# Optimization experiments

Hardware: AMD Instinct MI355X
Metric: run time of the kernel (lower is better)

Reference implementation:

```python
import jax, jax.numpy as jnp
from jax import lax
import numpy as np

B, T, F = 2048, 256, 64
HIDDEN = [64, 32, 16]
OUT = 1


def _lstm_params(key, in_dim, h):
    k1, k2, k3 = jax.random.split(key, 3)
    s_in = 1.0 / np.sqrt(in_dim)
    s_h = 1.0 / np.sqrt(h)
    W = jax.random.uniform(k1, (in_dim, 4 * h), jnp.float32, -s_in, s_in)
    U = jax.random.uniform(k2, (h, 4 * h), jnp.float32, -s_h, s_h)
    # Keras unit_forget_bias: bias starts at 0 except forget gate = 1
    b = jnp.concatenate([jnp.zeros((h,)), jnp.ones((h,)), jnp.zeros((2 * h,))]).astype(jnp.float32)
    return W, U, b


def setup_inputs() -> dict:
    key = jax.random.key(0)
    ks = jax.random.split(key, 6)
    x = jax.random.normal(ks[0], (B, T, F), jnp.float32)
    W0, U0, b0 = _lstm_params(ks[1], F, HIDDEN[0])
    W1, U1, b1 = _lstm_params(ks[2], HIDDEN[0], HIDDEN[1])
    W2, U2, b2 = _lstm_params(ks[3], HIDDEN[1], HIDDEN[2])
    s = 1.0 / np.sqrt(HIDDEN[2])
    Wd = jax.random.uniform(ks[4], (HIDDEN[2], OUT), jnp.float32, -s, s)
    bd = jnp.zeros((OUT,), jnp.float32)
    return {"x": x, "W0": W0, "U0": U0, "b0": b0,
            "W1": W1, "U1": U1, "b1": b1,
            "W2": W2, "U2": U2, "b2": b2,
            "Wd": Wd, "bd": bd}


def _lstm(x, W, U, b):
    """Keras-style LSTM scan. x: [B,T,in]. Returns (seq [B,T,H], last_h [B,H]).
    Gate order i,f,g,o; recurrent_activation=sigmoid, activation=tanh.
    Dropout/recurrent_dropout are identity at inference (training=False)."""
    Bsz = x.shape[0]
    H = U.shape[0]
    # precompute input projection for all timesteps (one big GEMM)
    xz = jnp.einsum('bti,ig->btg', x, W) + b  # [B,T,4H]
    xz_t = jnp.swapaxes(xz, 0, 1)  # [T,B,4H]

    def step(carry, z_in):
        h, c = carry
        z = z_in + h @ U  # [B,4H]
        i, f, g, o = jnp.split(z, 4, axis=-1)
        i = jax.nn.sigmoid(i)
        f = jax.nn.sigmoid(f)
        g = jnp.tanh(g)
        o = jax.nn.sigmoid(o)
        c = f * c + i * g
        h = o * jnp.tanh(c)
        return (h, c), h

    init = (jnp.zeros((Bsz, H), x.dtype), jnp.zeros((Bsz, H), x.dtype))
    (h_last, _), hs = lax.scan(step, init, xz_t)
    return jnp.swapaxes(hs, 0, 1), h_last


def reference(x, W0, U0, b0, W1, U1, b1, W2, U2, b2, Wd, bd):
    h, _ = _lstm(x, W0, U0, b0)          # return_sequences=True -> [B,T,64]
    h, _ = _lstm(h, W1, U1, b1)          # return_sequences=True -> [B,T,32]
    _, h_last = _lstm(h, W2, U2, b2)     # return_sequences=False -> [B,16]
    return h_last @ Wd + bd              # Dense -> [B,1]
```

## Files before the change

### kernel.cpp

```cpp
#include <hip/hip_runtime.h>


typedef __attribute__((ext_vector_type(8))) short s8v;
typedef __attribute__((ext_vector_type(4))) float f4v;
typedef unsigned short ushort_t;

#define T_STEPS 256
#define BT 8

#define XH  0
#define XL  2048
#define H0H 4096
#define H0L 6144
#define H1H 8192
#define H1L 9216
#define H2H 10240
#define H2L 11264
#define SM_SHORTS 12288

#define PIN(v) asm volatile("" : "+v"(v))
#define BAR()  asm volatile("s_waitcnt lgkmcnt(0)\n\ts_barrier" ::: "memory")

__device__ __forceinline__ unsigned short f2bf(float f) {
    unsigned u = __float_as_uint(f);
    u += 0x7fff + ((u >> 16) & 1);
    return (unsigned short)(u >> 16);
}
__device__ __forceinline__ float bf2f(unsigned short s) {
    return __uint_as_float(((unsigned)s) << 16);
}
__device__ __forceinline__ void tsplit(float v, unsigned short& hi, unsigned short& lo) {
    unsigned u = __float_as_uint(v);
    hi = (unsigned short)(u >> 16);
    float r = v - __uint_as_float(u & 0xffff0000u);
    lo = (unsigned short)(__float_as_uint(r) >> 16);
}
__device__ __forceinline__ float sigmoid_f(float x) {
    return __builtin_amdgcn_rcpf(1.0f + __expf(-x));
}
__device__ __forceinline__ float tanh_f(float x) {
    return 1.0f - 2.0f * __builtin_amdgcn_rcpf(__expf(2.0f * x) + 1.0f);
}

__device__ __forceinline__ float wval(const float* W, const float* U,
                                      int inDim, int KH, int fourH, int k, int n) {
    if (k < inDim) return W[k * fourH + n];
    if (k < KH)    return U[(k - inDim) * fourH + n];
    return 0.0f;
}
__device__ __forceinline__ void load_bfrag(const float* W, const float* U,
                                           int inDim, int KH, int fourH,
                                           int k0, int n, s8v& hi, s8v& lo) {
#pragma unroll
    for (int j = 0; j < 8; ++j) {
        float w = wval(W, U, inDim, KH, fourH, k0 + j, n);
        unsigned short h = f2bf(w);
        unsigned short l = f2bf(w - bf2f(h));
        hi[j] = (short)h;
        lo[j] = (short)l;
    }
}

__device__ __forceinline__ void gates2(const f4v* acc, bool low, float* c, float* hn) {
#pragma unroll
    for (int j = 0; j < 2; ++j) {
        float si = __shfl_xor(acc[0][j + 2], 32);
        float sf = __shfl_xor(acc[1][j + 2], 32);
        float sg = __shfl_xor(acc[2][j + 2], 32);
        float so = __shfl_xor(acc[3][j + 2], 32);
        float zi = low ? acc[0][j] : si;
        float zf = low ? acc[1][j] : sf;
        float zg = low ? acc[2][j] : sg;
        float zo = low ? acc[3][j] : so;
        float ig = sigmoid_f(zi);
        float fg = sigmoid_f(zf);
        float gg = tanh_f(zg);
        float og = sigmoid_f(zo);
        c[j] = fmaf(fg, c[j], ig * gg);
        hn[j] = og * tanh_f(c[j]);
    }
}

__global__ __attribute__((amdgpu_flat_work_group_size(512, 512),
                          amdgpu_waves_per_eu(2, 2)))
void lstm_pipe(const float* __restrict__ x,
               const float* __restrict__ W0, const float* __restrict__ U0, const float* __restrict__ b0,
               const float* __restrict__ W1, const float* __restrict__ U1, const float* __restrict__ b1,
               const float* __restrict__ W2, const float* __restrict__ U2, const float* __restrict__ b2,
               const float* __restrict__ Wd, const float* __restrict__ bd,
               float* __restrict__ out)
{
    const int tid  = threadIdx.x;
    const int lane = tid & 63;
    const int wv   = tid >> 6;
    const int fr   = lane >> 4;
    const int fc   = lane & 15;
    const int bbase = blockIdx.x * BT;

    __shared__ __align__(16) ushort_t SMEM[SM_SHORTS];
    __shared__ __align__(16) float h2last[BT][16];

    {
        unsigned* p32 = (unsigned*)SMEM;
        for (int i = tid; i < SM_SHORTS / 2; i += 512) p32[i] = 0u;
    }
    __syncthreads();

    const ushort_t* rb = SMEM + lane * 8;
    const bool low = (lane < 32);
    const int rowb = (fr & 1) * 4 + ((fr >> 1) << 1);

    if (wv < 4) {
        s8v Bh[4][4], Bl[4][4];
        float bias[4];
#pragma unroll
        for (int g = 0; g < 4; ++g) {
            int n = g * 64 + wv * 16 + fc;
            bias[g] = b0[n];
#pragma unroll
            for (int kc = 0; kc < 4; ++kc)
                load_bfrag(W0, U0, 64, 128, 256, kc * 32 + fr * 8, n, Bh[g][kc], Bl[g][kc]);
        }
#pragma unroll
        for (int g = 0; g < 4; ++g) {
            PIN(bias[g]);
#pragma unroll
            for (int kc = 0; kc < 4; ++kc) { PIN(Bh[g][kc]); PIN(Bl[g][kc]); }
        }
        float c0[2] = {0.f, 0.f};
        const int hq  = wv >> 1;
        const int k   = (wv & 1) * 16 + fc;
        const int ibw = (k >> 3) * 128 + (k & 7);
        __syncthreads();
        for (int s = 0; s < T_STEPS + 2; ++s) {
            if (s < T_STEPS) {
                const ushort_t* r = rb + ((s & 1) << 10);
                s8v ah[4], al[4];
                ah[0] = *(const s8v*)&r[XH  +   0];
                al[0] = *(const s8v*)&r[XL  +   0];
                ah[1] = *(const s8v*)&r[XH  + 512];
                al[1] = *(const s8v*)&r[XL  + 512];
                ah[2] = *(const s8v*)&r[H0H +   0];
                al[2] = *(const s8v*)&r[H0L +   0];
                ah[3] = *(const s8v*)&r[H0H + 512];
                al[3] = *(const s8v*)&r[H0L + 512];
                f4v acc[4];
#pragma unroll
                for (int g = 0; g < 4; ++g) acc[g] = (f4v){bias[g], bias[g], bias[g], bias[g]};
#pragma unroll
                for (int kc = 0; kc < 4; ++kc) {
#pragma unroll
                    for (int g = 0; g < 4; ++g)
                        acc[g] = __builtin_amdgcn_mfma_f32_16x16x32_bf16(ah[kc], Bh[g][kc], acc[g], 0, 0, 0);
#pragma unroll
                    for (int g = 0; g < 4; ++g)
                        acc[g] = __builtin_amdgcn_mfma_f32_16x16x32_bf16(al[kc], Bh[g][kc], acc[g], 0, 0, 0);
#pragma unroll
                    for (int g = 0; g < 4; ++g)
                        acc[g] = __builtin_amdgcn_mfma_f32_16x16x32_bf16(ah[kc], Bl[g][kc], acc[g], 0, 0, 0);
                }
                float hn[2];
                gates2(acc, low, c0, hn);
                {
                    ushort_t* w = SMEM + (((s & 1) ^ 1) << 10) + hq * 512 + ibw;
#pragma unroll
                    for (int j = 0; j < 2; ++j) {
                        unsigned short hh_, ll_;
                        tsplit(hn[j], hh_, ll_);
                        w[H0H + (rowb + j) * 8] = hh_;
                        w[H0L + (rowb + j) * 8] = ll_;
                    }
                }
            }
            BAR();
        }
    } else if (wv < 6) {
        s8v Bh[4][3], Bl[4][3];
        float bias[4];
#pragma unroll
        for (int g = 0; g < 4; ++g) {
            int n = g * 32 + (wv & 1) * 16 + fc;
            bias[g] = b1[n];
#pragma unroll
            for (int kc = 0; kc < 3; ++kc)
                load_bfrag(W1, U1, 64, 96, 128, kc * 32 + fr * 8, n, Bh[g][kc], Bl[g][kc]);
        }
#pragma unroll
        for (int g = 0; g < 4; ++g) {
            PIN(bias[g]);
#pragma unroll
            for (int kc = 0; kc < 3; ++kc) { PIN(Bh[g][kc]); PIN(Bl[g][kc]); }
        }
        float c1[2] = {0.f, 0.f};
        const int k   = (wv & 1) * 16 + fc;
        const int ibw = (k >> 3) * 128 + (k & 7);
        __syncthreads();
        for (int s = 0; s < T_STEPS + 2; ++s) {
            if (s >= 1 && s <= T_STEPS) {
                const int p = s & 1;
                const ushort_t* r  = rb + (p << 10);
                const ushort_t* r1 = rb + (p << 9);
                s8v ah[3], al[3];
                ah[0] = *(const s8v*)&r[H0H +   0];
                al[0] = *(const s8v*)&r[H0L +   0];
                ah[1] = *(const s8v*)&r[H0H + 512];
                al[1] = *(const s8v*)&r[H0L + 512];
                ah[2] = *(const s8v*)&r1[H1H];
                al[2] = *(const s8v*)&r1[H1L];
                f4v acc[4];
#pragma unroll
                for (int g = 0; g < 4; ++g) acc[g] = (f4v){bias[g], bias[g], bias[g], bias[g]};
#pragma unroll
                for (int kc = 0; kc < 3; ++kc) {
#pragma unroll
                    for (int g = 0; g < 4; ++g)
                        acc[g] = __builtin_amdgcn_mfma_f32_16x16x32_bf16(ah[kc], Bh[g][kc], acc[g], 0, 0, 0);
#pragma unroll
                    for (int g = 0; g < 4; ++g)
                        acc[g] = __builtin_amdgcn_mfma_f32_16x16x32_bf16(al[kc], Bh[g][kc], acc[g], 0, 0, 0);
#pragma unroll
                    for (int g = 0; g < 4; ++g)
                        acc[g] = __builtin_amdgcn_mfma_f32_16x16x32_bf16(ah[kc], Bl[g][kc], acc[g], 0, 0, 0);
                }
                float hn[2];
                gates2(acc, low, c1, hn);
                {
                    ushort_t* w = SMEM + ((p ^ 1) << 9) + ibw;
#pragma unroll
                    for (int j = 0; j < 2; ++j) {
                        unsigned short hh_, ll_;
                        tsplit(hn[j], hh_, ll_);
                        w[H1H + (rowb + j) * 8] = hh_;
                        w[H1L + (rowb + j) * 8] = ll_;
                    }
                }
            }
            BAR();
        }
    } else if (wv == 6) {
        s8v Bh[4][2], Bl[4][2];
        float bias[4];
#pragma unroll
        for (int g = 0; g < 4; ++g) {
            int n = g * 16 + fc;
            bias[g] = b2[n];
#pragma unroll
            for (int kc = 0; kc < 2; ++kc)
                load_bfrag(W2, U2, 32, 48, 64, kc * 32 + fr * 8, n, Bh[g][kc], Bl[g][kc]);
        }
#pragma unroll
        for (int g = 0; g < 4; ++g) {
            PIN(bias[g]);
#pragma unroll
            for (int kc = 0; kc < 2; ++kc) { PIN(Bh[g][kc]); PIN(Bl[g][kc]); }
        }
        float c2[2] = {0.f, 0.f};
        const int ibw = (fc >> 3) * 128 + (fc & 7);
        __syncthreads();
        for (int s = 0; s < T_STEPS + 2; ++s) {
            if (s >= 2) {
                const int p = s & 1;
                const ushort_t* r1 = rb + (p << 9);
                s8v ah[2], al[2];
                ah[0] = *(const s8v*)&r1[H1H];
                al[0] = *(const s8v*)&r1[H1L];
                ah[1] = *(const s8v*)&r1[H2H];
                al[1] = *(const s8v*)&r1[H2L];
                f4v acc[4];
#pragma unroll
                for (int g = 0; g < 4; ++g) acc[g] = (f4v){bias[g], bias[g], bias[g], bias[g]};
#pragma unroll
                for (int kc = 0; kc < 2; ++kc) {
#pragma unroll
                    for (int g = 0; g < 4; ++g)
                        acc[g] = __builtin_amdgcn_mfma_f32_16x16x32_bf16(ah[kc], Bh[g][kc], acc[g], 0, 0, 0);
#pragma unroll
                    for (int g = 0; g < 4; ++g)
                        acc[g] = __builtin_amdgcn_mfma_f32_16x16x32_bf16(al[kc], Bh[g][kc], acc[g], 0, 0, 0);
#pragma unroll
                    for (int g = 0; g < 4; ++g)
                        acc[g] = __builtin_amdgcn_mfma_f32_16x16x32_bf16(ah[kc], Bl[g][kc], acc[g], 0, 0, 0);
                }
                float hn[2];
                gates2(acc, low, c2, hn);
                {
                    ushort_t* w = SMEM + ((p ^ 1) << 9) + ibw;
#pragma unroll
                    for (int j = 0; j < 2; ++j) {
                        unsigned short hh_, ll_;
                        tsplit(hn[j], hh_, ll_);
                        w[H2H + (rowb + j) * 8] = hh_;
                        w[H2L + (rowb + j) * 8] = ll_;
                    }
                    if (s == T_STEPS + 1) {
#pragma unroll
                        for (int j = 0; j < 2; ++j) h2last[rowb + j][fc] = hn[j];
                    }
                }
            }
            BAR();
        }
    } else {
        const int xb = lane >> 3;
        const int fo = (lane & 7) * 8;
        const float* xp = x + ((size_t)(bbase + xb) * T_STEPS) * 64 + fo;
        const int o2 = (fo >> 5) * 512 + (((fo & 31) >> 3) * 16 + xb) * 8;

        auto write_x = [&](float4 v0, float4 v1, int tt) {
            float vv[8] = {v0.x, v0.y, v0.z, v0.w, v1.x, v1.y, v1.z, v1.w};
            s8v hi8, lo8;
#pragma unroll
            for (int j = 0; j < 8; ++j) {
                unsigned short h_, l_;
                tsplit(vv[j], h_, l_);
                hi8[j] = (short)h_;
                lo8[j] = (short)l_;
            }
            ushort_t* wbp = SMEM + ((tt & 1) << 10) + o2;
            *(s8v*)&wbp[XH] = hi8;
            *(s8v*)&wbp[XL] = lo8;
        };

        float4 pa = *(const float4*)(xp);
        float4 pb = *(const float4*)(xp + 4);
        write_x(pa, pb, 0);
        pa = *(const float4*)(xp + 64);
        pb = *(const float4*)(xp + 64 + 4);
        __syncthreads();
        for (int s = 0; s < T_STEPS + 2; ++s) {
            float4 na, nb;
            const bool ld = (s + 2 < T_STEPS);
            if (ld) {
                na = *(const float4*)(xp + (size_t)(s + 2) * 64);
                nb = *(const float4*)(xp + (size_t)(s + 2) * 64 + 4);
            }
            if (s + 1 < T_STEPS) write_x(pa, pb, s + 1);
            if (ld) { pa = na; pb = nb; }
            BAR();
        }
    }

    __syncthreads();
    if (tid < BT) {
        float acc = bd[0];
#pragma unroll
        for (int j = 0; j < 16; ++j) acc += h2last[tid][j] * Wd[j];
        out[bbase + tid] = acc;
    }
}

extern "C" void kernel_launch(void* const* d_in, const int* in_sizes, int n_in,
                              void* d_out, int out_size, void* d_ws, size_t ws_size,
                              hipStream_t stream) {
    (void)in_sizes; (void)n_in; (void)d_ws; (void)ws_size; (void)out_size;
    const float* x  = (const float*)d_in[0];
    const float* W0 = (const float*)d_in[1];
    const float* U0 = (const float*)d_in[2];
    const float* b0 = (const float*)d_in[3];
    const float* W1 = (const float*)d_in[4];
    const float* U1 = (const float*)d_in[5];
    const float* b1 = (const float*)d_in[6];
    const float* W2 = (const float*)d_in[7];
    const float* U2 = (const float*)d_in[8];
    const float* b2 = (const float*)d_in[9];
    const float* Wd = (const float*)d_in[10];
    const float* bd = (const float*)d_in[11];
    float* out = (float*)d_out;

    dim3 grid(2048 / BT);
    dim3 block(512);
    hipLaunchKernelGGL(lstm_pipe, grid, block, 0, stream,
                       x, W0, U0, b0, W1, U1, b1, W2, U2, b2, Wd, bd, out);
}
```

Measured before the change: 416.6 us.

## Move layer-0 input projection into loader waves, staging gate preactivations in LDS

```diff
diff --git a/kernel.cpp b/kernel.cpp
--- a/kernel.cpp
+++ b/kernel.cpp
@@ -8,15 +8,13 @@
 #define T_STEPS 256
 #define BT 8
 
-#define XH  0
-#define XL  2048
-#define H0H 4096
-#define H0L 6144
-#define H1H 8192
-#define H1L 9216
-#define H2H 10240
-#define H2L 11264
-#define SM_SHORTS 12288
+#define H0H 0
+#define H0L 2048
+#define H1H 4096
+#define H1L 5120
+#define H2H 6144
+#define H2L 7168
+#define SM_SHORTS 8192
 
 #define PIN(v) asm volatile("" : "+v"(v))
 #define BAR()  asm volatile("s_waitcnt lgkmcnt(0)\n\ts_barrier" ::: "memory")
@@ -81,6 +79,32 @@
     }
 }
 
+template<int CG0>
+__device__ __forceinline__ void produce8(const s8v* axh, const s8v* axl,
+                                         const float* bw, int pcpar,
+                                         int lane, int fr, int fc,
+                                         ushort_t* w0s, float* zx)
+{
+    const int woff = (pcpar << 12) + ((fr >> 1) << 11) + ((fr & 1) << 2);
+#pragma unroll
+    for (int i = 0; i < 8; ++i) {
+        const int cg = CG0 + i;
+        const int col = cg * 16 + fc;
+        const float bv = bw[cg];
+        f4v acc = (f4v){bv, bv, bv, bv};
+#pragma unroll
+        for (int kc = 0; kc < 2; ++kc) {
+            const int fb = ((cg * 2 + kc) << 9) + lane * 8;
+            s8v bh = *(const s8v*)&w0s[fb];
+            s8v bl = *(const s8v*)&w0s[16384 + fb];
+            acc = __builtin_amdgcn_mfma_f32_16x16x32_bf16(axh[kc], bh, acc, 0, 0, 0);
+            acc = __builtin_amdgcn_mfma_f32_16x16x32_bf16(axl[kc], bh, acc, 0, 0, 0);
+            acc = __builtin_amdgcn_mfma_f32_16x16x32_bf16(axh[kc], bl, acc, 0, 0, 0);
+        }
+        *(f4v*)&zx[woff + col * 8] = acc;
+    }
+}
+
 __global__ __attribute__((amdgpu_flat_work_group_size(512, 512),
                           amdgpu_waves_per_eu(2, 2)))
 void lstm_pipe(const float* __restrict__ x,
@@ -98,12 +122,25 @@
     const int bbase = blockIdx.x * BT;
 
     __shared__ __align__(16) ushort_t SMEM[SM_SHORTS];
+    __shared__ __align__(16) float    ZX[8192];
+    __shared__ __align__(16) ushort_t W0S[32768];
     __shared__ __align__(16) float h2last[BT][16];
 
     {
         unsigned* p32 = (unsigned*)SMEM;
         for (int i = tid; i < SM_SHORTS / 2; i += 512) p32[i] = 0u;
     }
+    for (int it = tid; it < 16384; it += 512) {
+        const int n = it & 255;
+        const int k = it >> 8;
+        const float w = W0[it];
+        const int kc = k >> 5, kfr = (k >> 3) & 3, j = k & 7;
+        const int cg = n >> 4, nfc = n & 15;
+        const int pos = ((cg * 2 + kc) * 64 + (kfr * 16 + nfc)) * 8 + j;
+        unsigned short h = f2bf(w);
+        W0S[pos] = h;
+        W0S[16384 + pos] = f2bf(w - bf2f(h));
+    }
     __syncthreads();
 
     const ushort_t* rb = SMEM + lane * 8;
@@ -111,54 +148,53 @@
     const int rowb = (fr & 1) * 4 + ((fr >> 1) << 1);
 
     if (wv < 4) {
-        s8v Bh[4][4], Bl[4][4];
-        float bias[4];
+        s8v Bh[4][2], Bl[4][2];
 #pragma unroll
         for (int g = 0; g < 4; ++g) {
             int n = g * 64 + wv * 16 + fc;
-            bias[g] = b0[n];
-#pragma unroll
-            for (int kc = 0; kc < 4; ++kc)
-                load_bfrag(W0, U0, 64, 128, 256, kc * 32 + fr * 8, n, Bh[g][kc], Bl[g][kc]);
-        }
-#pragma unroll
-        for (int g = 0; g < 4; ++g) {
-            PIN(bias[g]);
-#pragma unroll
-            for (int kc = 0; kc < 4; ++kc) { PIN(Bh[g][kc]); PIN(Bl[g][kc]); }
-        }
+#pragma unroll
+            for (int kc = 0; kc < 2; ++kc)
+                load_bfrag(U0, U0, 64, 64, 256, kc * 32 + fr * 8, n, Bh[g][kc], Bl[g][kc]);
+        }
+#pragma unroll
+        for (int g = 0; g < 4; ++g)
+#pragma unroll
+            for (int kc = 0; kc < 2; ++kc) { PIN(Bh[g][kc]); PIN(Bl[g][kc]); }
         float c0[2] = {0.f, 0.f};
         const int hq  = wv >> 1;
         const int k   = (wv & 1) * 16 + fc;
         const int ibw = (k >> 3) * 128 + (k & 7);
+        const int zb  = (wv * 16 + fc) * 8 + ((fr & 1) << 2);
         __syncthreads();
         for (int s = 0; s < T_STEPS + 2; ++s) {
             if (s < T_STEPS) {
                 const ushort_t* r = rb + ((s & 1) << 10);
-                s8v ah[4], al[4];
-                ah[0] = *(const s8v*)&r[XH  +   0];
-                al[0] = *(const s8v*)&r[XL  +   0];
-                ah[1] = *(const s8v*)&r[XH  + 512];
-                al[1] = *(const s8v*)&r[XL  + 512];
-                ah[2] = *(const s8v*)&r[H0H +   0];
-                al[2] = *(const s8v*)&r[H0L +   0];
-                ah[3] = *(const s8v*)&r[H0H + 512];
-                al[3] = *(const s8v*)&r[H0L + 512];
+                s8v ah0 = *(const s8v*)&r[H0H +   0];
+                s8v al0 = *(const s8v*)&r[H0L +   0];
+                s8v ah1 = *(const s8v*)&r[H0H + 512];
+                s8v al1 = *(const s8v*)&r[H0L + 512];
+                const float* zr = ZX + ((((s >> 1) & 1) << 12) + ((s & 1) << 11) + zb);
                 f4v acc[4];
 #pragma unroll
-                for (int g = 0; g < 4; ++g) acc[g] = (f4v){bias[g], bias[g], bias[g], bias[g]};
-#pragma unroll
-                for (int kc = 0; kc < 4; ++kc) {
-#pragma unroll
-                    for (int g = 0; g < 4; ++g)
-                        acc[g] = __builtin_amdgcn_mfma_f32_16x16x32_bf16(ah[kc], Bh[g][kc], acc[g], 0, 0, 0);
-#pragma unroll
-                    for (int g = 0; g < 4; ++g)
-                        acc[g] = __builtin_amdgcn_mfma_f32_16x16x32_bf16(al[kc], Bh[g][kc], acc[g], 0, 0, 0);
-#pragma unroll
-                    for (int g = 0; g < 4; ++g)
-                        acc[g] = __builtin_amdgcn_mfma_f32_16x16x32_bf16(ah[kc], Bl[g][kc], acc[g], 0, 0, 0);
-                }
+                for (int g = 0; g < 4; ++g) acc[g] = *(const f4v*)&zr[g * 512];
+#pragma unroll
+                for (int g = 0; g < 4; ++g)
+                    acc[g] = __builtin_amdgcn_mfma_f32_16x16x32_bf16(ah0, Bh[g][0], acc[g], 0, 0, 0);
+#pragma unroll
+                for (int g = 0; g < 4; ++g)
+                    acc[g] = __builtin_amdgcn_mfma_f32_16x16x32_bf16(al0, Bh[g][0], acc[g], 0, 0, 0);
+#pragma unroll
+                for (int g = 0; g < 4; ++g)
+                    acc[g] = __builtin_amdgcn_mfma_f32_16x16x32_bf16(ah0, Bl[g][0], acc[g], 0, 0, 0);
+#pragma unroll
+                for (int g = 0; g < 4; ++g)
+                    acc[g] = __builtin_amdgcn_mfma_f32_16x16x32_bf16(ah1, Bh[g][1], acc[g], 0, 0, 0);
+#pragma unroll
+                for (int g = 0; g < 4; ++g)
+                    acc[g] = __builtin_amdgcn_mfma_f32_16x16x32_bf16(al1, Bh[g][1], acc[g], 0, 0, 0);
+#pragma unroll
+                for (int g = 0; g < 4; ++g)
+                    acc[g] = __builtin_amdgcn_mfma_f32_16x16x32_bf16(ah1, Bl[g][1], acc[g], 0, 0, 0);
                 float hn[2];
                 gates2(acc, low, c0, hn);
                 {
@@ -301,41 +337,62 @@
             BAR();
         }
     } else {
-        const int xb = lane >> 3;
-        const int fo = (lane & 7) * 8;
-        const float* xp = x + ((size_t)(bbase + xb) * T_STEPS) * 64 + fo;
-        const int o2 = (fo >> 5) * 512 + (((fo & 31) >> 3) * 16 + xb) * 8;
-
-        auto write_x = [&](float4 v0, float4 v1, int tt) {
-            float vv[8] = {v0.x, v0.y, v0.z, v0.w, v1.x, v1.y, v1.z, v1.w};
-            s8v hi8, lo8;
-#pragma unroll
-            for (int j = 0; j < 8; ++j) {
-                unsigned short h_, l_;
-                tsplit(vv[j], h_, l_);
-                hi8[j] = (short)h_;
-                lo8[j] = (short)l_;
+        float bw[16];
+#pragma unroll
+        for (int cg = 0; cg < 16; ++cg) bw[cg] = b0[cg * 16 + fc];
+        const int tl = fc >> 3;
+        const float* xlane = x + ((size_t)(bbase + (fc & 7)) * T_STEPS) * 64 + fr * 8;
+
+        auto xload = [&](int cc, float4* rx) {
+            const float* p = xlane + (size_t)(cc * 2 + tl) * 64;
+            rx[0] = *(const float4*)(p);
+            rx[1] = *(const float4*)(p + 4);
+            rx[2] = *(const float4*)(p + 32);
+            rx[3] = *(const float4*)(p + 36);
+        };
+        auto dotsplit = [&](const float4* rx, s8v* axh, s8v* axl) {
+#pragma unroll
+            for (int kc = 0; kc < 2; ++kc) {
+                float vv[8] = {rx[kc*2].x, rx[kc*2].y, rx[kc*2].z, rx[kc*2].w,
+                               rx[kc*2+1].x, rx[kc*2+1].y, rx[kc*2+1].z, rx[kc*2+1].w};
+#pragma unroll
+                for (int j = 0; j < 8; ++j) {
+                    unsigned short h_, l_;
+                    tsplit(vv[j], h_, l_);
+                    axh[kc][j] = (short)h_;
+                    axl[kc][j] = (short)l_;
+                }
             }
-            ushort_t* wbp = SMEM + ((tt & 1) << 10) + o2;
-            *(s8v*)&wbp[XH] = hi8;
-            *(s8v*)&wbp[XL] = lo8;
         };
 
-        float4 pa = *(const float4*)(xp);
-        float4 pb = *(const float4*)(xp + 4);
-        write_x(pa, pb, 0);
-        pa = *(const float4*)(xp + 64);
-        pb = *(const float4*)(xp + 64 + 4);
+        s8v axh[2], axl[2];
+        float4 rxA[4], rxB[4], rt[4];
+        xload(0, rt);
+        dotsplit(rt, axh, axl);
+        produce8<0>(axh, axl, bw, 0, lane, fr, fc, W0S, ZX);
+        produce8<8>(axh, axl, bw, 0, lane, fr, fc, W0S, ZX);
+        xload(1, rt);
+        dotsplit(rt, axh, axl);
+        xload(2, rxA);
         __syncthreads();
         for (int s = 0; s < T_STEPS + 2; ++s) {
-            float4 na, nb;
-            const bool ld = (s + 2 < T_STEPS);
-            if (ld) {
-                na = *(const float4*)(xp + (size_t)(s + 2) * 64);
-                nb = *(const float4*)(xp + (size_t)(s + 2) * 64 + 4);
+            if (s < 2 * 127) {
+                const int c = s >> 1;
+                const int pcpar = (c + 1) & 1;
+                if ((s & 1) == 0) {
+                    produce8<0>(axh, axl, bw, pcpar, lane, fr, fc, W0S, ZX);
+                } else {
+                    produce8<8>(axh, axl, bw, pcpar, lane, fr, fc, W0S, ZX);
+                    if (c + 2 <= 127) {
+                        if ((c & 1) == 0) dotsplit(rxA, axh, axl);
+                        else              dotsplit(rxB, axh, axl);
+                    }
+                    if (c + 3 <= 127) {
+                        if ((c & 1) == 0) xload(c + 3, rxB);
+                        else              xload(c + 3, rxA);
+                    }
+                }
             }
-            if (s + 1 < T_STEPS) write_x(pa, pb, s + 1);
-            if (ld) { pa = na; pb = nb; }
             BAR();
         }
     }
```

After: 559.7 us. 1.34x slower.
